# Optimization experiments

Measured on AMD Instinct MI355X. Metric: run time of the kernel, lower is better.

## Reference

```python
import jax, jax.numpy as jnp
import numpy as np

EMBED = 256
HEADS = 8
HD = EMBED // HEADS
LEVELS = 4
POINTS = 4
FFN_H = 1024
BS = 8
LQ = 900
SHAPES = [(100, 100), (50, 50), (25, 25), (13, 13)]


def setup_inputs() -> dict:
    key = jax.random.key(0)
    ks = jax.random.split(key, 20)
    nv = sum(h * w for h, w in SHAPES)
    starts = np.cumsum([0] + [h * w for h, w in SHAPES])[:-1]
    inp = {
        "queries": jax.random.normal(ks[0], (BS, LQ, EMBED), jnp.float32),
        "memory": jax.random.normal(ks[1], (BS, nv, EMBED), jnp.float32),
        "query_pos": jax.random.normal(ks[2], (BS, LQ, EMBED), jnp.float32),
        "reference_points": jax.random.uniform(ks[3], (BS, LQ, LEVELS, 4), jnp.float32) * 0.9 + 0.05,
        "spatial_shapes": jnp.asarray(SHAPES, jnp.int32),
        "level_start_index": jnp.asarray(starts, jnp.int32),
    }
    def lin(k, din, dout):
        k1, k2 = jax.random.split(k)
        w = jax.random.normal(k1, (din, dout), jnp.float32) * 0.02
        b = jax.random.normal(k2, (dout,), jnp.float32) * 0.01
        return w, b
    specs = [("Wq", "bq", EMBED, EMBED), ("Wk", "bk", EMBED, EMBED), ("Wv", "bv", EMBED, EMBED),
             ("Wo", "bo", EMBED, EMBED), ("Wvd", "bvd", EMBED, EMBED),
             ("Woff", "boff", EMBED, HEADS * LEVELS * POINTS * 2),
             ("Watt", "batt", EMBED, HEADS * LEVELS * POINTS),
             ("Wop", "bop", EMBED, EMBED), ("Wg", "bg", 2 * EMBED, 2 * EMBED),
             ("W1", "b1", EMBED, FFN_H), ("W2", "b2", FFN_H, EMBED)]
    for i, (wn, bn, di, do) in enumerate(specs):
        w, b = lin(ks[4 + i], di, do)
        inp[wn] = w
        inp[bn] = b
    for n in ["ln1", "ln2", "ln3"]:
        inp[n + "_s"] = jnp.ones((EMBED,), jnp.float32)
        inp[n + "_b"] = jnp.zeros((EMBED,), jnp.float32)
    return inp


def _ln(x, s, b):
    m = jnp.mean(x, -1, keepdims=True)
    v = jnp.mean(jnp.square(x - m), -1, keepdims=True)
    return (x - m) * jax.lax.rsqrt(v + 1e-5) * s + b


def _bilinear(v_l, lx, ly, H, W):
    # v_l: [bs,h,H*W,hd]; lx,ly: [bs,h,lq,p] normalized in [0,1]
    # grid_sample(align_corners=False, padding=zeros) semantics
    px = lx * W - 0.5
    py = ly * H - 0.5
    x0 = jnp.floor(px)
    y0 = jnp.floor(py)
    wx = px - x0
    wy = py - y0
    x0i = x0.astype(jnp.int32)
    y0i = y0.astype(jnp.int32)
    bs, h, lq, p = lx.shape
    out = jnp.zeros((bs, h, lq, p, HD), v_l.dtype)
    for dy in (0, 1):
        for dx in (0, 1):
            xi = x0i + dx
            yi = y0i + dy
            w = (wx if dx else 1.0 - wx) * (wy if dy else 1.0 - wy)
            valid = (xi >= 0) & (xi < W) & (yi >= 0) & (yi < H)
            idx = jnp.clip(yi, 0, H - 1) * W + jnp.clip(xi, 0, W - 1)
            g = jnp.take_along_axis(v_l, idx.reshape(bs, h, lq * p)[..., None], axis=2)
            g = g.reshape(bs, h, lq, p, HD)
            out = out + w[..., None] * jnp.where(valid[..., None], g, 0.0)
    return out


def reference(queries, memory, query_pos, reference_points, spatial_shapes, level_start_index,
              Wq, bq, Wk, bk, Wv, bv, Wo, bo, Wvd, bvd, Woff, boff, Watt, batt, Wop, bop,
              Wg, bg, W1, b1, W2, b2, ln1_s, ln1_b, ln2_s, ln2_b, ln3_s, ln3_b):
    bs, lq, _ = queries.shape
    shp = np.asarray(spatial_shapes)
    st = np.asarray(level_start_index)

    # ---- self attention (pre-norm, q=k=x+pos, v=x) ----
    x = _ln(queries, ln1_s, ln1_b)
    qk = x + query_pos
    Q = (qk @ Wq + bq).reshape(bs, lq, HEADS, HD)
    K = (qk @ Wk + bk).reshape(bs, lq, HEADS, HD)
    V = (x @ Wv + bv).reshape(bs, lq, HEADS, HD)
    scores = jnp.einsum('bqhd,bkhd->bhqk', Q, K) * (1.0 / np.sqrt(HD))
    attn = jax.nn.softmax(scores, axis=-1)
    sa = jnp.einsum('bhqk,bkhd->bqhd', attn, V).reshape(bs, lq, EMBED) @ Wo + bo
    x1 = queries + sa  # dropout is identity in eval

    # ---- MS-deformable cross attention ----
    y = _ln(x1, ln2_s, ln2_b)
    qc = y + query_pos
    val = (memory @ Wvd + bvd).reshape(bs, -1, HEADS, HD).transpose(0, 2, 1, 3)  # [bs,h,Nv,hd]
    off = (qc @ Woff + boff).reshape(bs, lq, HEADS, LEVELS, POINTS, 2)
    aw = jax.nn.softmax((qc @ Watt + batt).reshape(bs, lq, HEADS, LEVELS * POINTS), axis=-1)
    aw = aw.reshape(bs, lq, HEADS, LEVELS, POINTS)
    rp = reference_points[:, :, None, :, None, :]  # [bs,lq,1,L,1,4]
    loc = rp[..., :2] + off / POINTS * rp[..., 2:] * 0.5  # [bs,lq,h,L,p,2]

    out = jnp.zeros((bs, HEADS, lq, HD), queries.dtype)
    for l in range(LEVELS):
        H, W = int(shp[l, 0]), int(shp[l, 1])
        s0 = int(st[l])
        v_l = val[:, :, s0:s0 + H * W]
        lx = jnp.transpose(loc[:, :, :, l, :, 0], (0, 2, 1, 3))  # [bs,h,lq,p]
        ly = jnp.transpose(loc[:, :, :, l, :, 1], (0, 2, 1, 3))
        samp = _bilinear(v_l, lx, ly, H, W)  # [bs,h,lq,p,hd]
        w = jnp.transpose(aw[:, :, :, l], (0, 2, 1, 3))  # [bs,h,lq,p]
        out = out + jnp.sum(w[..., None] * samp, axis=3)
    cross = out.transpose(0, 2, 1, 3).reshape(bs, lq, EMBED) @ Wop + bop

    # ---- gated fusion ----
    gi = jnp.concatenate([x1, cross], axis=-1)
    g = jax.nn.sigmoid(gi @ Wg + bg)
    x2 = g[..., :EMBED] * x1 + g[..., EMBED:] * cross

    # ---- FFN ----
    z = _ln(x2, ln3_s, ln3_b)
    ffn = jax.nn.relu(z @ W1 + b1) @ W2 + b2
    return (x2 + ffn, aw, loc)
```

## Files before the change

### kernel.cpp

```cpp
#include <hip/hip_runtime.h>
#include <hip/hip_bf16.h>
#include <math.h>

#define BB 8
#define LQ 900
#define EE 256
#define NH 8
#define HD 32
#define NL 4
#define NP 4
#define FFN_H 1024

typedef __bf16 bf16x8 __attribute__((ext_vector_type(8)));
typedef float f32x4 __attribute__((ext_vector_type(4)));
typedef unsigned short u16x8 __attribute__((ext_vector_type(8)));

__device__ __forceinline__ unsigned short f2b(float f) {
    union { float f; unsigned int u; } v; v.f = f;
    unsigned int u = v.u;
    unsigned int r = (u + 0x7fffu + ((u >> 16) & 1u)) >> 16;
    return (unsigned short)r;
}
__device__ __forceinline__ float b2f(unsigned short h) {
    union { unsigned int u; float f; } v; v.u = ((unsigned int)h) << 16; return v.f;
}

typedef __attribute__((address_space(3))) unsigned int* lds_ptr_t;
typedef const __attribute__((address_space(1))) unsigned int* gbl_ptr_t;
#define GLOAD16(g, l) __builtin_amdgcn_global_load_lds((gbl_ptr_t)(g), (lds_ptr_t)(l), 16, 0, 0)
#define VMCNT(n) asm volatile("s_waitcnt vmcnt(" #n ")" ::: "memory")

struct TDesc { const float* src; unsigned short* dst; int K, N, tile0; };
struct TPack {
    TDesc d[12];
    const float *bq, *bk, *boff, *batt;
    float *bqk, *boa;
    const float *Wop_src, *Wg_src, *bop_src, *bg_src;
    unsigned short* WopRow;
    float* bgg;
};

__global__ __launch_bounds__(256) void prep_kernel(
    TPack p,
    const float* __restrict__ queries, const float* __restrict__ qpos,
    const float* __restrict__ ln1_s, const float* __restrict__ ln1_b,
    unsigned short* __restrict__ x_b, unsigned short* __restrict__ qk_b,
    const float* __restrict__ mem, unsigned short* __restrict__ mem_b, long memN)
{
    const int bi = blockIdx.x;
    const int t = threadIdx.x;

    if (bi < 1248) {
        int di = 0;
#pragma unroll
        for (int i = 1; i < 12; ++i) if (bi >= p.d[i].tile0) di = i;
        TDesc d = p.d[di];
        int tt = bi - d.tile0;
        int tn = (d.N + 31) >> 5;
        int tk = tt / tn, tc = tt % tn;
        __shared__ float tile[32][33];
        int tx = t & 31, ty = t >> 5;
#pragma unroll
        for (int i = 0; i < 4; ++i) {
            int kk = tk * 32 + ty + i * 8, nn = tc * 32 + tx;
            tile[ty + i * 8][tx] = d.src[(size_t)kk * d.N + nn];
        }
        __syncthreads();
#pragma unroll
        for (int i = 0; i < 4; ++i) {
            int nn = tc * 32 + ty + i * 8, kk = tk * 32 + tx;
            d.dst[(size_t)nn * d.K + kk] = f2b(tile[tx][ty + i * 8]);
        }
        return;
    }
    if (bi < 1252) {
        int which = bi - 1248;
        if (which == 0)      p.bqk[t] = p.bq[t];
        else if (which == 1) p.bqk[256 + t] = p.bk[t];
        else if (which == 2) p.boa[t] = p.boff[t];
        else if (t < 128)    p.boa[256 + t] = p.batt[t];
        return;
    }
    if (bi < 1284) {
        long i = ((long)(bi - 1252) * 256 + t) * 8;
        float4 a = *(const float4*)(p.Wop_src + i);
        float4 b = *(const float4*)(p.Wop_src + i + 4);
        u16x8 o;
        o[0] = f2b(a.x); o[1] = f2b(a.y); o[2] = f2b(a.z); o[3] = f2b(a.w);
        o[4] = f2b(b.x); o[5] = f2b(b.y); o[6] = f2b(b.z); o[7] = f2b(b.w);
        *(u16x8*)(p.WopRow + i) = o;
        return;
    }
    if (bi < 1286) {
        int n = (bi - 1284) * 256 + t;
        float bb = p.bg_src[n];
        for (int j = 0; j < 256; ++j)
            bb += p.bop_src[j] * p.Wg_src[(size_t)(256 + j) * 512 + n];
        p.bgg[n] = bb;
        return;
    }
    if (bi < 8486) {
        const int row = bi - 1286;
        const int w = t >> 6, lane = t & 63;
        __shared__ float red[4];
        float v = queries[(size_t)row * EE + t];
        float sum = v;
#pragma unroll
        for (int o = 32; o; o >>= 1) sum += __shfl_xor(sum, o, 64);
        if (lane == 0) red[w] = sum;
        __syncthreads();
        float mean = (red[0] + red[1] + red[2] + red[3]) * (1.0f / 256.0f);
        __syncthreads();
        float dd = v - mean;
        float sq = dd * dd;
#pragma unroll
        for (int o = 32; o; o >>= 1) sq += __shfl_xor(sq, o, 64);
        if (lane == 0) red[w] = sq;
        __syncthreads();
        float var = (red[0] + red[1] + red[2] + red[3]) * (1.0f / 256.0f);
        float y = dd * rsqrtf(var + 1e-5f) * ln1_s[t] + ln1_b[t];
        x_b[(size_t)row * EE + t]  = f2b(y);
        qk_b[(size_t)row * EE + t] = f2b(y + qpos[(size_t)row * EE + t]);
        return;
    }
    {
        long i = ((long)(bi - 8486) * 256 + t) * 8;
        long stride = (long)2048 * 256 * 8;
        for (; i < memN; i += stride) {
            float4 a = *(const float4*)(mem + i);
            float4 b = *(const float4*)(mem + i + 4);
            u16x8 o;
            o[0] = f2b(a.x); o[1] = f2b(a.y); o[2] = f2b(a.z); o[3] = f2b(a.w);
            o[4] = f2b(b.x); o[5] = f2b(b.y); o[6] = f2b(b.z); o[7] = f2b(b.w);
            *(u16x8*)(mem_b + i) = o;
        }
    }
}

struct GD {
    const unsigned short* A;
    const unsigned short* Bt;
    const float* bias;
    const float* resid;
    float* outF;
    unsigned short* outB;
    const float* lnS; const float* lnB; const float* lnAdd;
    unsigned short* lnOut;
    int M, K, N, ntN, tile0, ldOutB, outBoff, act, ldA;
};
struct GB { GD d[4]; int nd, tot; };

template<int BN>
__global__ __launch_bounds__(256, (BN == 128) ? 4 : 2) void gemm_pipe(GB g) {
    constexpr int STAGES = (BN == 128) ? 3 : 2;
    __shared__ __align__(16) unsigned short ldsb[STAGES][(64 + BN) * 32];
    __shared__ float lnred[2][64][2];
    const int tid = threadIdx.x;
    const int l = tid & 63, w = tid >> 6;
    const int wr = w >> 1, wc = w & 1;
    constexpr int NJ = BN / 32;

    int t = blockIdx.x;
    if (t >= g.tot) return;
    int d = 0;
    while (d + 1 < g.nd && t >= g.d[d + 1].tile0) ++d;

    auto stage = [&](int dd, int tt, int ks, int pp) {
        const GD& D = g.d[dd];
        const int lda = D.ldA ? D.ldA : D.K;
        int local = tt - D.tile0;
        int m0 = (local / D.ntN) * 64;
        int n0 = (local % D.ntN) * BN;
        unsigned short* base = &ldsb[pp][0];
        {
            int row = w * 16 + (l >> 2);
            int rg = m0 + row; int mm = D.M - 1; rg = rg < mm ? rg : mm;
            int schunk = ((l & 3) ^ ((row >> 1) & 3)) << 4;
            GLOAD16((const char*)(D.A + (size_t)rg * lda + (ks << 5)) + schunk,
                    base + (w * 16) * 32);
        }
#pragma unroll
        for (int ib = 0; ib < BN / 64; ++ib) {
            int row = ib * 64 + w * 16 + (l >> 2);
            int rg = n0 + row; int nn = D.N - 1; rg = rg < nn ? rg : nn;
            int schunk = ((l & 3) ^ ((row >> 1) & 3)) << 4;
            GLOAD16((const char*)(D.Bt + (size_t)rg * D.K + (ks << 5)) + schunk,
                    base + 2048 + (ib * 64 + w * 16) * 32);
        }
    };

    int st_t = t, st_ks = 0, st_d = d;
    bool st_valid = true;
    auto advance = [&]() {
        ++st_ks;
        if (st_ks == (g.d[st_d].K >> 5)) {
            st_ks = 0;
            st_t += gridDim.x;
            if (st_t >= g.tot) { st_valid = false; }
            else { while (st_d + 1 < g.nd && st_t >= g.d[st_d + 1].tile0) ++st_d; }
        }
    };

    int sp = 0, cp = 0, nf = 0;
    stage(st_d, st_t, st_ks, sp); sp = (sp + 1 == STAGES) ? 0 : sp + 1; ++nf; advance();
    if (STAGES == 3 && st_valid) {
        stage(st_d, st_t, st_ks, sp); sp = (sp + 1 == STAGES) ? 0 : sp + 1; ++nf; advance();
    }

    while (true) {
        const GD D = g.d[d];
        int local = t - D.tile0;
        const int m0 = (local / D.ntN) * 64;
        const int n0 = (local % D.ntN) * BN;
        const int nk = D.K >> 5;

        f32x4 acc[2][NJ];
#pragma unroll
        for (int i = 0; i < 2; ++i)
#pragma unroll
            for (int j = 0; j < NJ; ++j) acc[i][j] = (f32x4){0.f, 0.f, 0.f, 0.f};

        for (int ks = 0; ks < nk; ++ks) {
            if (st_valid && nf < STAGES) {
                stage(st_d, st_t, st_ks, sp);
                sp = (sp + 1 == STAGES) ? 0 : sp + 1;
                ++nf; advance();
            }
            if (nf == 3)      { VMCNT(6); }
            else if (nf == 2) { if constexpr (BN == 128) { VMCNT(3); } else { VMCNT(5); } }
            else              { VMCNT(0); }
            __builtin_amdgcn_sched_barrier(0);
            __builtin_amdgcn_s_barrier();
            __builtin_amdgcn_sched_barrier(0);
            {
                const char* base = (const char*)&ldsb[cp][0];
                const int rch = ((l >> 4) ^ ((l >> 1) & 3)) << 4;
                bf16x8 af[2];
#pragma unroll
                for (int i = 0; i < 2; ++i) {
                    int row = wr * 32 + i * 16 + (l & 15);
                    af[i] = *(const bf16x8*)(base + row * 64 + rch);
                }
#pragma unroll
                for (int j = 0; j < NJ; ++j) {
                    int row = wc * (BN / 2) + j * 16 + (l & 15);
                    bf16x8 bfr = *(const bf16x8*)(base + 4096 + row * 64 + rch);
#pragma unroll
                    for (int i = 0; i < 2; ++i)
                        acc[i][j] = __builtin_amdgcn_mfma_f32_16x16x32_bf16(af[i], bfr, acc[i][j], 0, 0, 0);
                }
            }
            __builtin_amdgcn_sched_barrier(0);
            __builtin_amdgcn_s_barrier();
            __builtin_amdgcn_sched_barrier(0);
            cp = (cp + 1 == STAGES) ? 0 : cp + 1;
            --nf;
        }

#pragma unroll
        for (int i = 0; i < 2; ++i) {
#pragma unroll
            for (int r = 0; r < 4; ++r) {
                int gm = m0 + wr * 32 + i * 16 + ((l >> 4) << 2) + r;
                if (gm >= D.M) continue;
#pragma unroll
                for (int j = 0; j < NJ; ++j) {
                    int gn = n0 + wc * (BN / 2) + j * 16 + (l & 15);
                    if (gn >= D.N) continue;
                    float v = acc[i][j][r];
                    if (D.bias)  v += D.bias[gn];
                    if (D.resid) v += D.resid[(size_t)gm * D.N + gn];
                    if (D.act == 1)      v = fmaxf(v, 0.f);
                    else if (D.act == 2) v = 1.0f / (1.0f + __expf(-v));
                    acc[i][j][r] = v;
                    if (D.outF) D.outF[(size_t)gm * D.N + gn] = v;
                    if (D.outB) D.outB[(size_t)gm * D.ldOutB + D.outBoff + gn] = f2b(v);
                }
            }
        }

        if constexpr (BN == 256) {
            if (D.lnOut) {
#pragma unroll
                for (int i = 0; i < 2; ++i) {
#pragma unroll
                    for (int r = 0; r < 4; ++r) {
                        float s1 = 0.f, s2 = 0.f;
#pragma unroll
                        for (int j = 0; j < NJ; ++j) {
                            float v = acc[i][j][r];
                            s1 += v; s2 += v * v;
                        }
#pragma unroll
                        for (int o = 1; o <= 8; o <<= 1) {
                            s1 += __shfl_xor(s1, o, 64);
                            s2 += __shfl_xor(s2, o, 64);
                        }
                        if ((l & 15) == 0) {
                            int row = wr * 32 + i * 16 + ((l >> 4) << 2) + r;
                            lnred[wc][row][0] = s1;
                            lnred[wc][row][1] = s2;
                        }
                    }
                }
                __syncthreads();
#pragma unroll
                for (int i = 0; i < 2; ++i) {
#pragma unroll
                    for (int r = 0; r < 4; ++r) {
                        int row = wr * 32 + i * 16 + ((l >> 4) << 2) + r;
                        int gm = m0 + row;
                        if (gm >= D.M) continue;
                        float mean = (lnred[0][row][0] + lnred[1][row][0]) * (1.0f / 256.0f);
                        float msq  = (lnred[0][row][1] + lnred[1][row][1]) * (1.0f / 256.0f);
                        float rs = rsqrtf(msq - mean * mean + 1e-5f);
#pragma unroll
                        for (int j = 0; j < NJ; ++j) {
                            int gn = wc * 128 + j * 16 + (l & 15);
                            float y = (acc[i][j][r] - mean) * rs * D.lnS[gn] + D.lnB[gn]
                                      + D.lnAdd[(size_t)gm * 256 + gn];
                            D.lnOut[(size_t)gm * 256 + gn] = f2b(y);
                        }
                    }
                }
            }
        }

        t += gridDim.x;
        if (t >= g.tot) break;
        while (d + 1 < g.nd && t >= g.d[d + 1].tile0) ++d;
    }
}

__global__ __launch_bounds__(256) void attn_mfma(
    const unsigned short* __restrict__ QK, const unsigned short* __restrict__ Vb,
    unsigned short* __restrict__ outB)
{
    const int qt = blockIdx.x;
    const int bh = blockIdx.y;
    const int b = bh >> 3, h = bh & 7;
    const int tid = threadIdx.x;
    const int w = tid >> 6, l = tid & 63;

    __shared__ __align__(16) unsigned short Ks[64 * 32];
    __shared__ __align__(16) unsigned short VT[32 * 64];
    __shared__ __align__(16) unsigned short Ps[4][64 * 20];

    const int qrow_w = qt * 64 + w * 16;
    int qr = qrow_w + (l & 15); qr = qr < LQ ? qr : LQ - 1;
    bf16x8 qf = *(const bf16x8*)(QK + ((size_t)(b * LQ + qr)) * 512 + h * 32 + (l >> 4) * 8);

    f32x4 acc0 = {0.f, 0.f, 0.f, 0.f}, acc1 = {0.f, 0.f, 0.f, 0.f};
    float m_run = -1e30f, l_run = 0.f;
    const float scale = 0.17677669529663689f;
    const f32x4 z4 = {0.f, 0.f, 0.f, 0.f};

    const int key = tid >> 2;
    const int dg = (tid & 3) * 8;
    u16x8 kvc, vvc, kvn, vvn;
    {
        int krow = key; krow = krow < LQ ? krow : LQ - 1;
        size_t base = (size_t)(b * LQ + krow);
        kvc = *(const u16x8*)(QK + base * 512 + 256 + h * 32 + dg);
        vvc = *(const u16x8*)(Vb + base * 256 + h * 32 + dg);
    }

    for (int kt = 0; kt < 15; ++kt) {
        __syncthreads();
        *(u16x8*)((char*)Ks + key * 64 + ((dg * 2) ^ ((key & 3) << 4))) = kvc;
#pragma unroll
        for (int e = 0; e < 8; ++e) {
            int dd = dg + e;
            *(unsigned short*)((char*)VT + dd * 128 + ((key * 2) ^ ((dd & 7) << 4))) = vvc[e];
        }
        if (kt < 14) {
            int krow = (kt + 1) * 64 + key; krow = krow < LQ ? krow : LQ - 1;
            size_t base = (size_t)(b * LQ + krow);
            kvn = *(const u16x8*)(QK + base * 512 + 256 + h * 32 + dg);
            vvn = *(const u16x8*)(Vb + base * 256 + h * 32 + dg);
        }
        __syncthreads();

        float p[4][4];
        float tmax = -1e30f;
#pragma unroll
        for (int m = 0; m < 4; ++m) {
            int kr = m * 16 + (l & 15);
            bf16x8 kf = *(const bf16x8*)((const char*)Ks + kr * 64 +
                        (((l >> 4) * 16) ^ ((kr & 3) << 4)));
            f32x4 sf = __builtin_amdgcn_mfma_f32_16x16x32_bf16(kf, qf, z4, 0, 0, 0);
#pragma unroll
            for (int r = 0; r < 4; ++r) {
                int kk = kt * 64 + m * 16 + (l >> 4) * 4 + r;
                float sv = (kk < LQ) ? sf[r] * scale : -1e30f;
                p[m][r] = sv;
                tmax = fmaxf(tmax, sv);
            }
        }
        tmax = fmaxf(tmax, __shfl_xor(tmax, 16, 64));
        tmax = fmaxf(tmax, __shfl_xor(tmax, 32, 64));
        float newm = fmaxf(m_run, tmax);
        float corr = __expf(m_run - newm);
        m_run = newm;
        float tsum = 0.f;
#pragma unroll
        for (int m = 0; m < 4; ++m)
#pragma unroll
            for (int r = 0; r < 4; ++r) {
                float e = __expf(p[m][r] - newm);
                p[m][r] = e;
                tsum += e;
            }
        tsum += __shfl_xor(tsum, 16, 64);
        tsum += __shfl_xor(tsum, 32, 64);
        l_run = l_run * corr + tsum;
        acc0 *= corr;
        acc1 *= corr;

        unsigned short* pw = &Ps[w][0];
#pragma unroll
        for (int m = 0; m < 4; ++m)
#pragma unroll
            for (int r = 0; r < 4; ++r) {
                int kk = m * 16 + (l >> 4) * 4 + r;
                pw[kk * 20 + (l & 15)] = f2b(p[m][r]);
            }

#pragma unroll
        for (int s = 0; s < 2; ++s) {
            union { unsigned short u[8]; bf16x8 v; } pb;
#pragma unroll
            for (int j = 0; j < 8; ++j)
                pb.u[j] = pw[(s * 32 + (l >> 4) * 8 + j) * 20 + (l & 15)];
#pragma unroll
            for (int m2 = 0; m2 < 2; ++m2) {
                int dd = m2 * 16 + (l & 15);
                bf16x8 vf = *(const bf16x8*)((const char*)VT + dd * 128 +
                            ((s * 64 + (l >> 4) * 16) ^ ((dd & 7) << 4)));
                if (m2 == 0) acc0 = __builtin_amdgcn_mfma_f32_16x16x32_bf16(vf, pb.v, acc0, 0, 0, 0);
                else         acc1 = __builtin_amdgcn_mfma_f32_16x16x32_bf16(vf, pb.v, acc1, 0, 0, 0);
            }
        }
        if (kt < 14) { kvc = kvn; vvc = vvn; }
    }

    float inv = 1.0f / l_run;
    int q = qrow_w + (l & 15);
    if (q < LQ) {
        size_t obase = ((size_t)(b * LQ + q)) * 256 + h * 32;
#pragma unroll
        for (int r = 0; r < 4; ++r) {
            int d0 = (l >> 4) * 4 + r;
            outB[obase + d0]      = f2b(acc0[r] * inv);
            outB[obase + 16 + d0] = f2b(acc1[r] * inv);
        }
    }
}

__global__ __launch_bounds__(256) void sample_fused(
    const float* __restrict__ off_att, const float* __restrict__ refp,
    const unsigned short* __restrict__ val,
    const int* __restrict__ shapes, const int* __restrict__ starts,
    float* __restrict__ aw_out, float* __restrict__ loc_out,
    unsigned short* __restrict__ xs, int NV)
{
    const int row = blockIdx.x;
    const int b = row / LQ;
    const int t = threadIdx.x;
    const int h = t >> 5, d = t & 31;

    __shared__ float l_logit[128];
    __shared__ float l_aw[128];
    __shared__ float l_loc[256];
    __shared__ int l_sh[NL * 2];
    __shared__ int l_st[NL];

    if (t < 128) l_logit[t] = off_att[(size_t)row * 384 + 256 + t];
    {
        float o = off_att[(size_t)row * 384 + t];
        int c = t & 1;
        int lv = (t >> 3) & 3;
        float rc = refp[((size_t)row * 4 + lv) * 4 + c];
        float rs = refp[((size_t)row * 4 + lv) * 4 + 2 + c];
        float loc = rc + o * 0.125f * rs;
        l_loc[t] = loc;
        loc_out[(size_t)row * 256 + t] = loc;
    }
    if (t < NL * 2) l_sh[t] = shapes[t];
    if (t < NL) l_st[t] = starts[t];
    __syncthreads();
    if (t < 128) {
        int hh = t >> 4;
        float mx = -1e30f;
#pragma unroll
        for (int i = 0; i < 16; ++i) mx = fmaxf(mx, l_logit[hh * 16 + i]);
        float sum = 0.f;
#pragma unroll
        for (int i = 0; i < 16; ++i) sum += __expf(l_logit[hh * 16 + i] - mx);
        float aw = __expf(l_logit[t] - mx) / sum;
        l_aw[t] = aw;
        aw_out[(size_t)row * 128 + t] = aw;
    }
    __syncthreads();

    float acc = 0.f;
    const unsigned short* vb = val + (size_t)b * NV * EE + h * HD + d;

#pragma unroll
    for (int lv = 0; lv < NL; ++lv) {
        const int Hh = l_sh[lv * 2], Ww = l_sh[lv * 2 + 1];
        const int s0 = l_st[lv];
#pragma unroll
        for (int p = 0; p < NP; ++p) {
            const int base = ((h * NL + lv) * NP + p) * 2;
            float lx = l_loc[base], ly = l_loc[base + 1];
            float wgt0 = l_aw[h * 16 + lv * NP + p];
            float px = lx * (float)Ww - 0.5f;
            float py = ly * (float)Hh - 0.5f;
            float x0f = floorf(px), y0f = floorf(py);
            float wx = px - x0f, wy = py - y0f;
            int x0 = (int)x0f, y0 = (int)y0f;
#pragma unroll
            for (int dy = 0; dy < 2; ++dy) {
                int yi = y0 + dy;
                bool vy = (yi >= 0) && (yi < Hh);
                int yc = min(max(yi, 0), Hh - 1);
                float wyv = dy ? wy : 1.f - wy;
#pragma unroll
                for (int dx = 0; dx < 2; ++dx) {
                    int xi = x0 + dx;
                    bool vv = vy && (xi >= 0) && (xi < Ww);
                    int xc = min(max(xi, 0), Ww - 1);
                    float wgt = wgt0 * wyv * (dx ? wx : 1.f - wx);
                    float gv = b2f(vb[(size_t)(s0 + yc * Ww + xc) * EE]);
                    acc += vv ? wgt * gv : 0.f;
                }
            }
        }
    }
    xs[(size_t)row * 512 + 256 + t] = f2b(acc);
}

__global__ __launch_bounds__(256) void gate_ln3(
    const float* __restrict__ g, const float* __restrict__ x1,
    const float* __restrict__ cross, const float* __restrict__ s,
    const float* __restrict__ bln, float* __restrict__ x2out,
    unsigned short* __restrict__ zb)
{
    const int row = blockIdx.x;
    const int t = threadIdx.x;
    const int w = t >> 6;
    const int lane = t & 63;
    __shared__ float red[4];

    float g1 = g[(size_t)row * 512 + t];
    float g2 = g[(size_t)row * 512 + 256 + t];
    float v = g1 * x1[(size_t)row * EE + t] + g2 * cross[(size_t)row * EE + t];
    x2out[(size_t)row * EE + t] = v;

    float sum = v;
#pragma unroll
    for (int o = 32; o; o >>= 1) sum += __shfl_xor(sum, o, 64);
    if (lane == 0) red[w] = sum;
    __syncthreads();
    float mean = (red[0] + red[1] + red[2] + red[3]) * (1.0f / 256.0f);
    __syncthreads();

    float d = v - mean;
    float sq = d * d;
#pragma unroll
    for (int o = 32; o; o >>= 1) sq += __shfl_xor(sq, o, 64);
    if (lane == 0) red[w] = sq;
    __syncthreads();
    float var = (red[0] + red[1] + red[2] + red[3]) * (1.0f / 256.0f);

    float y = d * rsqrtf(var + 1e-5f) * s[t] + bln[t];
    zb[(size_t)row * EE + t] = f2b(y);
}

extern "C" void kernel_launch(void* const* d_in, const int* in_sizes, int n_in,
                              void* d_out, int out_size, void* d_ws, size_t ws_size,
                              hipStream_t stream)
{
    const float* queries   = (const float*)d_in[0];
    const float* memory    = (const float*)d_in[1];
    const float* query_pos = (const float*)d_in[2];
    const float* refp      = (const float*)d_in[3];
    const int*   shapes    = (const int*)d_in[4];
    const int*   starts    = (const int*)d_in[5];
    const float* Wq  = (const float*)d_in[6],  *bq  = (const float*)d_in[7];
    const float* Wk  = (const float*)d_in[8],  *bk  = (const float*)d_in[9];
    const float* Wv  = (const float*)d_in[10], *bv  = (const float*)d_in[11];
    const float* Wo  = (const float*)d_in[12], *bo  = (const float*)d_in[13];
    const float* Wvd = (const float*)d_in[14], *bvd = (const float*)d_in[15];
    const float* Woff= (const float*)d_in[16], *boff= (const float*)d_in[17];
    const float* Watt= (const float*)d_in[18], *batt= (const float*)d_in[19];
    const float* Wop = (const float*)d_in[20], *bop = (const float*)d_in[21];
    const float* Wg  = (const float*)d_in[22], *bg  = (const float*)d_in[23];
    const float* W1  = (const float*)d_in[24], *b1  = (const float*)d_in[25];
    const float* W2  = (const float*)d_in[26], *b2  = (const float*)d_in[27];
    const float* ln1_s = (const float*)d_in[28], *ln1_b = (const float*)d_in[29];
    const float* ln2_s = (const float*)d_in[30], *ln2_b = (const float*)d_in[31];
    const float* ln3_s = (const float*)d_in[32], *ln3_b = (const float*)d_in[33];

    const int NV = in_sizes[1] / (BB * EE);
    const int Mq = BB * LQ;
    const int Mv = BB * NV;
    const long memN = (long)Mv * EE;

    char* W8 = (char*)d_ws;
    size_t off = 0;
    auto alloc = [&](size_t bytes) { char* p = W8 + off; off += (bytes + 255) & ~(size_t)255; return p; };

    unsigned short* mem_b = (unsigned short*)alloc((size_t)memN * 2);
    unsigned short* val_b = (unsigned short*)alloc((size_t)memN * 2);
    unsigned short* WtQK  = (unsigned short*)alloc(512 * 256 * 2);
    unsigned short* WtV   = (unsigned short*)alloc(256 * 256 * 2);
    unsigned short* WtO   = (unsigned short*)alloc(256 * 256 * 2);
    unsigned short* WtVD  = (unsigned short*)alloc(256 * 256 * 2);
    unsigned short* WtOA  = (unsigned short*)alloc(384 * 256 * 2);
    unsigned short* WtOP  = (unsigned short*)alloc(256 * 256 * 2);
    unsigned short* WtGF  = (unsigned short*)alloc(512 * 512 * 2);
    unsigned short* Wg2T  = (unsigned short*)alloc(512 * 256 * 2);
    unsigned short* WopRow= (unsigned short*)alloc(256 * 256 * 2);
    unsigned short* Wt1   = (unsigned short*)alloc(1024 * 256 * 2);
    unsigned short* Wt2   = (unsigned short*)alloc(256 * 1024 * 2);
    float*          bqk   = (float*)alloc(512 * 4);
    float*          boa   = (float*)alloc(384 * 4);
    float*          bgg   = (float*)alloc(512 * 4);
    unsigned short* qkb   = (unsigned short*)alloc((size_t)Mq * 512 * 2);
    unsigned short* vb_buf= (unsigned short*)alloc((size_t)Mq * 256 * 2);
    unsigned short* av_buf= (unsigned short*)alloc((size_t)Mq * 256 * 2);
    float*          x1    = (float*)alloc((size_t)Mq * 256 * 4);
    unsigned short* xs_cat= (unsigned short*)alloc((size_t)Mq * 512 * 2);
    unsigned short* qc_b  = (unsigned short*)alloc((size_t)Mq * 256 * 2);
    unsigned short* qk_b  = (unsigned short*)alloc((size_t)Mq * 256 * 2);
    float*          cross = (float*)alloc((size_t)Mq * 256 * 4);

    unsigned short* x_b = (unsigned short*)cross;
    float* off_att = (float*)qkb;
    float* gbuf = (float*)mem_b;
    float* x2   = (float*)((char*)mem_b + (size_t)Mq * 512 * 4);
    unsigned short* z_b = (unsigned short*)((char*)x2 + (size_t)Mq * 256 * 4);
    unsigned short* hidden_b = (unsigned short*)((char*)z_b + (size_t)Mq * 256 * 2);

    float* out0    = (float*)d_out;
    float* aw_out  = out0 + (size_t)Mq * 256;
    float* loc_out = aw_out + (size_t)Mq * 128;

    dim3 blk(256);
    const int tMq = (Mq + 63) / 64;
    const int tv  = (Mv + 63) / 64;

    TPack tp;
    tp.d[0]  = { Wq,             WtQK,             256, 256,    0 };
    tp.d[1]  = { Wk,             WtQK + 256 * 256, 256, 256,   64 };
    tp.d[2]  = { Wv,             WtV,              256, 256,  128 };
    tp.d[3]  = { Wo,             WtO,              256, 256,  192 };
    tp.d[4]  = { Wvd,            WtVD,             256, 256,  256 };
    tp.d[5]  = { Woff,           WtOA,             256, 256,  320 };
    tp.d[6]  = { Watt,           WtOA + 256 * 256, 256, 128,  384 };
    tp.d[7]  = { Wop,            WtOP,             256, 256,  416 };
    tp.d[8]  = { Wg,             WtGF,             512, 512,  480 };
    tp.d[9]  = { Wg + 256 * 512, Wg2T,             256, 512,  608 };
    tp.d[10] = { W1,             Wt1,              256, 1024, 736 };
    tp.d[11] = { W2,             Wt2,             1024, 256,  992 };
    tp.bq = bq; tp.bk = bk; tp.boff = boff; tp.batt = batt;
    tp.bqk = bqk; tp.boa = boa;
    tp.Wop_src = Wop; tp.Wg_src = Wg; tp.bop_src = bop; tp.bg_src = bg;
    tp.WopRow = WopRow; tp.bgg = bgg;
    prep_kernel<<<10534, blk, 0, stream>>>(
        tp, queries, query_pos, ln1_s, ln1_b, x_b, qk_b, memory, mem_b, memN);

    {
        GB g; g.nd = 4;
        g.d[0] = { mem_b, WtVD, bvd, nullptr, nullptr, val_b,
                   nullptr, nullptr, nullptr, nullptr,
                   Mv, 256, 256, 2, 0, 256, 0, 0, 0 };
        g.d[1] = { qk_b, WtQK, bqk, nullptr, nullptr, qkb,
                   nullptr, nullptr, nullptr, nullptr,
                   Mq, 256, 512, 4, tv * 2, 512, 0, 0, 0 };
        g.d[2] = { x_b, WtV, bv, nullptr, nullptr, vb_buf,
                   nullptr, nullptr, nullptr, nullptr,
                   Mq, 256, 256, 2, tv * 2 + tMq * 4, 256, 0, 0, 0 };
        g.d[3] = { Wg2T, WopRow, nullptr, nullptr, nullptr, WtGF,
                   nullptr, nullptr, nullptr, nullptr,
                   512, 256, 256, 2, tv * 2 + tMq * 6, 512, 256, 0, 0 };
        g.tot = tv * 2 + tMq * 6 + 16;
        gemm_pipe<128><<<1536, blk, 0, stream>>>(g);
    }

    attn_mfma<<<dim3(15, BB * NH), blk, 0, stream>>>(qkb, vb_buf, av_buf);

    {
        GB g; g.nd = 1;
        g.d[0] = { av_buf, WtO, bo, queries, x1, xs_cat,
                   ln2_s, ln2_b, query_pos, qc_b,
                   Mq, 256, 256, 1, 0, 512, 0, 0, 0 };
        g.tot = tMq;
        gemm_pipe<256><<<tMq, blk, 0, stream>>>(g);
    }

    {
        GB g; g.nd = 1;
        g.d[0] = { qc_b, WtOA, boa, nullptr, off_att, nullptr,
                   nullptr, nullptr, nullptr, nullptr,
                   Mq, 256, 384, 3, 0, 384, 0, 0, 0 };
        g.tot = tMq * 3;
        gemm_pipe<128><<<g.tot, blk, 0, stream>>>(g);
    }

    sample_fused<<<Mq, blk, 0, stream>>>(off_att, refp, val_b, shapes, starts,
                                         aw_out, loc_out, xs_cat, NV);

    {
        GB g; g.nd = 2;
        g.d[0] = { xs_cat + 256, WtOP, bop, nullptr, cross, nullptr,
                   nullptr, nullptr, nullptr, nullptr,
                   Mq, 256, 256, 2, 0, 0, 0, 0, 512 };
        g.d[1] = { xs_cat, WtGF, bgg, nullptr, gbuf, nullptr,
                   nullptr, nullptr, nullptr, nullptr,
                   Mq, 512, 512, 4, tMq * 2, 0, 0, 2, 0 };
        g.tot = tMq * 6;
        gemm_pipe<128><<<g.tot, blk, 0, stream>>>(g);
    }

    gate_ln3<<<Mq, blk, 0, stream>>>(gbuf, x1, cross, ln3_s, ln3_b, x2, z_b);

    {
        GB g; g.nd = 1;
        g.d[0] = { z_b, Wt1, b1, nullptr, nullptr, hidden_b,
                   nullptr, nullptr, nullptr, nullptr,
                   Mq, 256, 1024, 8, 0, 1024, 0, 1, 0 };
        g.tot = tMq * 8;
        gemm_pipe<128><<<g.tot, blk, 0, stream>>>(g);
    }

    {
        GB g; g.nd = 1;
        g.d[0] = { hidden_b, Wt2, b2, x2, out0, nullptr,
                   nullptr, nullptr, nullptr, nullptr,
                   Mq, 1024, 256, 2, 0, 256, 0, 0, 0 };
        g.tot = tMq * 2;
        gemm_pipe<128><<<g.tot, blk, 0, stream>>>(g);
    }
}
```

Measured before the change: 346.4 us.

## Co-schedule value projection GEMM with self-attention kernel and simplify GEMM pipeline

The large memory value-projection GEMM moves out of the batched projection launch and into the self-attention launch. Extra blocks in that launch run it as a persistent double-buffered GEMM, so it overlaps with the attention blocks instead of sitting ahead of them. The generic GEMM kernel drops its 3-stage cross-tile prefetch for a simpler 2-stage double buffer. This cuts LDS use and may raise occupancy, but it risks less latency hiding. Shared memory in the attention kernel is merged into one buffer that both block roles reuse.

```diff
diff --git a/kernel.cpp b/kernel.cpp
--- a/kernel.cpp
+++ b/kernel.cpp
@@ -148,12 +148,11 @@
     unsigned short* lnOut;
     int M, K, N, ntN, tile0, ldOutB, outBoff, act, ldA;
 };
-struct GB { GD d[4]; int nd, tot; };
+struct GB { GD d[3]; int nd, tot; };
 
 template<int BN>
 __global__ __launch_bounds__(256, (BN == 128) ? 4 : 2) void gemm_pipe(GB g) {
-    constexpr int STAGES = (BN == 128) ? 3 : 2;
-    __shared__ __align__(16) unsigned short ldsb[STAGES][(64 + BN) * 32];
+    __shared__ __align__(16) unsigned short ldsb[2][(64 + BN) * 32];
     __shared__ float lnred[2][64][2];
     const int tid = threadIdx.x;
     const int l = tid & 63, w = tid >> 6;
@@ -189,23 +188,8 @@
         }
     };
 
-    int st_t = t, st_ks = 0, st_d = d;
-    bool st_valid = true;
-    auto advance = [&]() {
-        ++st_ks;
-        if (st_ks == (g.d[st_d].K >> 5)) {
-            st_ks = 0;
-            st_t += gridDim.x;
-            if (st_t >= g.tot) { st_valid = false; }
-            else { while (st_d + 1 < g.nd && st_t >= g.d[st_d + 1].tile0) ++st_d; }
-        }
-    };
-
-    int sp = 0, cp = 0, nf = 0;
-    stage(st_d, st_t, st_ks, sp); sp = (sp + 1 == STAGES) ? 0 : sp + 1; ++nf; advance();
-    if (STAGES == 3 && st_valid) {
-        stage(st_d, st_t, st_ks, sp); sp = (sp + 1 == STAGES) ? 0 : sp + 1; ++nf; advance();
-    }
+    stage(d, t, 0, 0);
+    int p = 0;
 
     while (true) {
         const GD D = g.d[d];
@@ -221,19 +205,24 @@
             for (int j = 0; j < NJ; ++j) acc[i][j] = (f32x4){0.f, 0.f, 0.f, 0.f};
 
         for (int ks = 0; ks < nk; ++ks) {
-            if (st_valid && nf < STAGES) {
-                stage(st_d, st_t, st_ks, sp);
-                sp = (sp + 1 == STAGES) ? 0 : sp + 1;
-                ++nf; advance();
-            }
-            if (nf == 3)      { VMCNT(6); }
-            else if (nf == 2) { if constexpr (BN == 128) { VMCNT(3); } else { VMCNT(5); } }
-            else              { VMCNT(0); }
+            int nt = t, nks = ks + 1, ndd = d;
+            bool have = true;
+            if (nks == nk) {
+                nt = t + gridDim.x; nks = 0;
+                if (nt >= g.tot) have = false;
+                else { while (ndd + 1 < g.nd && nt >= g.d[ndd + 1].tile0) ++ndd; }
+            }
+            if (have) {
+                stage(ndd, nt, nks, p ^ 1);
+                if constexpr (BN == 128) { VMCNT(3); } else { VMCNT(5); }
+            } else {
+                VMCNT(0);
+            }
             __builtin_amdgcn_sched_barrier(0);
             __builtin_amdgcn_s_barrier();
             __builtin_amdgcn_sched_barrier(0);
             {
-                const char* base = (const char*)&ldsb[cp][0];
+                const char* base = (const char*)&ldsb[p][0];
                 const int rch = ((l >> 4) ^ ((l >> 1) & 3)) << 4;
                 bf16x8 af[2];
 #pragma unroll
@@ -253,8 +242,7 @@
             __builtin_amdgcn_sched_barrier(0);
             __builtin_amdgcn_s_barrier();
             __builtin_amdgcn_sched_barrier(0);
-            cp = (cp + 1 == STAGES) ? 0 : cp + 1;
-            --nf;
+            p ^= 1;
         }
 
 #pragma unroll
@@ -332,19 +320,122 @@
     }
 }
 
-__global__ __launch_bounds__(256) void attn_mfma(
+#define VGRID 1536
+
+__global__ __launch_bounds__(256) void attn_val(
     const unsigned short* __restrict__ QK, const unsigned short* __restrict__ Vb,
-    unsigned short* __restrict__ outB)
+    unsigned short* __restrict__ outB,
+    const unsigned short* __restrict__ vA, const unsigned short* __restrict__ vBt,
+    const float* __restrict__ vbias, unsigned short* __restrict__ vout,
+    int Mv, int vtiles)
 {
-    const int qt = blockIdx.x;
-    const int bh = blockIdx.y;
+    __shared__ __align__(16) unsigned short smem[(64 + 128) * 32 * 2];
+    const int bid = blockIdx.x;
+    const int tid = threadIdx.x;
+    const int l = tid & 63, w = tid >> 6;
+
+    if (bid >= 960) {
+        const int wr = w >> 1, wc = w & 1;
+        int t = bid - 960;
+        if (t >= vtiles) return;
+
+        auto stage = [&](int tt, int ks, int pp) {
+            unsigned short* base = &smem[pp * 192 * 32];
+            int m0 = (tt >> 1) * 64;
+            int n0 = (tt & 1) * 128;
+            {
+                int row = w * 16 + (l >> 2);
+                int rg = m0 + row; int mm = Mv - 1; rg = rg < mm ? rg : mm;
+                int schunk = ((l & 3) ^ ((row >> 1) & 3)) << 4;
+                GLOAD16((const char*)(vA + (size_t)rg * 256 + (ks << 5)) + schunk,
+                        base + (w * 16) * 32);
+            }
+#pragma unroll
+            for (int ib = 0; ib < 2; ++ib) {
+                int row = ib * 64 + w * 16 + (l >> 2);
+                int rg = n0 + row;
+                int schunk = ((l & 3) ^ ((row >> 1) & 3)) << 4;
+                GLOAD16((const char*)(vBt + (size_t)rg * 256 + (ks << 5)) + schunk,
+                        base + 2048 + (ib * 64 + w * 16) * 32);
+            }
+        };
+
+        stage(t, 0, 0);
+        int p = 0;
+        while (true) {
+            const int m0 = (t >> 1) * 64;
+            const int n0 = (t & 1) * 128;
+
+            f32x4 acc[2][4];
+#pragma unroll
+            for (int i = 0; i < 2; ++i)
+#pragma unroll
+                for (int j = 0; j < 4; ++j) acc[i][j] = (f32x4){0.f, 0.f, 0.f, 0.f};
+
+            for (int ks = 0; ks < 8; ++ks) {
+                int nt = t, nks = ks + 1;
+                bool have = true;
+                if (nks == 8) {
+                    nt = t + VGRID; nks = 0;
+                    if (nt >= vtiles) have = false;
+                }
+                if (have) { stage(nt, nks, p ^ 1); VMCNT(3); }
+                else      { VMCNT(0); }
+                __builtin_amdgcn_sched_barrier(0);
+                __builtin_amdgcn_s_barrier();
+                __builtin_amdgcn_sched_barrier(0);
+                {
+                    const char* base = (const char*)&smem[p * 192 * 32];
+                    const int rch = ((l >> 4) ^ ((l >> 1) & 3)) << 4;
+                    bf16x8 af[2];
+#pragma unroll
+                    for (int i = 0; i < 2; ++i) {
+                        int row = wr * 32 + i * 16 + (l & 15);
+                        af[i] = *(const bf16x8*)(base + row * 64 + rch);
+                    }
+#pragma unroll
+                    for (int j = 0; j < 4; ++j) {
+                        int row = wc * 64 + j * 16 + (l & 15);
+                        bf16x8 bfr = *(const bf16x8*)(base + 4096 + row * 64 + rch);
+#pragma unroll
+                        for (int i = 0; i < 2; ++i)
+                            acc[i][j] = __builtin_amdgcn_mfma_f32_16x16x32_bf16(af[i], bfr, acc[i][j], 0, 0, 0);
+                    }
+                }
+                __builtin_amdgcn_sched_barrier(0);
+                __builtin_amdgcn_s_barrier();
+                __builtin_amdgcn_sched_barrier(0);
+                p ^= 1;
+            }
+
+#pragma unroll
+            for (int i = 0; i < 2; ++i) {
+#pragma unroll
+                for (int r = 0; r < 4; ++r) {
+                    int gm = m0 + wr * 32 + i * 16 + ((l >> 4) << 2) + r;
+                    if (gm >= Mv) continue;
+#pragma unroll
+                    for (int j = 0; j < 4; ++j) {
+                        int gn = n0 + wc * 64 + j * 16 + (l & 15);
+                        float v = acc[i][j][r] + vbias[gn];
+                        vout[(size_t)gm * 256 + gn] = f2b(v);
+                    }
+                }
+            }
+
+            t += VGRID;
+            if (t >= vtiles) break;
+        }
+        return;
+    }
+
+    const int qt = bid % 15;
+    const int bh = bid / 15;
     const int b = bh >> 3, h = bh & 7;
-    const int tid = threadIdx.x;
-    const int w = tid >> 6, l = tid & 63;
-
-    __shared__ __align__(16) unsigned short Ks[64 * 32];
-    __shared__ __align__(16) unsigned short VT[32 * 64];
-    __shared__ __align__(16) unsigned short Ps[4][64 * 20];
+
+    unsigned short* Ks = smem;
+    unsigned short* VT = smem + 2048;
+    unsigned short* Ps = smem + 4096;
 
     const int qrow_w = qt * 64 + w * 16;
     int qr = qrow_w + (l & 15); qr = qr < LQ ? qr : LQ - 1;
@@ -381,7 +472,7 @@
         }
         __syncthreads();
 
-        float p[4][4];
+        float pv[4][4];
         float tmax = -1e30f;
 #pragma unroll
         for (int m = 0; m < 4; ++m) {
@@ -393,7 +484,7 @@
             for (int r = 0; r < 4; ++r) {
                 int kk = kt * 64 + m * 16 + (l >> 4) * 4 + r;
                 float sv = (kk < LQ) ? sf[r] * scale : -1e30f;
-                p[m][r] = sv;
+                pv[m][r] = sv;
                 tmax = fmaxf(tmax, sv);
             }
         }
@@ -407,8 +498,8 @@
         for (int m = 0; m < 4; ++m)
 #pragma unroll
             for (int r = 0; r < 4; ++r) {
-                float e = __expf(p[m][r] - newm);
-                p[m][r] = e;
+                float e = __expf(pv[m][r] - newm);
+                pv[m][r] = e;
                 tsum += e;
             }
         tsum += __shfl_xor(tsum, 16, 64);
@@ -417,13 +508,13 @@
         acc0 *= corr;
         acc1 *= corr;
 
-        unsigned short* pw = &Ps[w][0];
+        unsigned short* pw = Ps + w * 1280;
 #pragma unroll
         for (int m = 0; m < 4; ++m)
 #pragma unroll
             for (int r = 0; r < 4; ++r) {
                 int kk = m * 16 + (l >> 4) * 4 + r;
-                pw[kk * 20 + (l & 15)] = f2b(p[m][r]);
+                pw[kk * 20 + (l & 15)] = f2b(pv[m][r]);
             }
 
 #pragma unroll
@@ -673,24 +764,22 @@
         tp, queries, query_pos, ln1_s, ln1_b, x_b, qk_b, memory, mem_b, memN);
 
     {
-        GB g; g.nd = 4;
-        g.d[0] = { mem_b, WtVD, bvd, nullptr, nullptr, val_b,
+        GB g; g.nd = 3;
+        g.d[0] = { qk_b, WtQK, bqk, nullptr, nullptr, qkb,
                    nullptr, nullptr, nullptr, nullptr,
-                   Mv, 256, 256, 2, 0, 256, 0, 0, 0 };
-        g.d[1] = { qk_b, WtQK, bqk, nullptr, nullptr, qkb,
+                   Mq, 256, 512, 4, 0, 512, 0, 0, 0 };
+        g.d[1] = { x_b, WtV, bv, nullptr, nullptr, vb_buf,
                    nullptr, nullptr, nullptr, nullptr,
-                   Mq, 256, 512, 4, tv * 2, 512, 0, 0, 0 };
-        g.d[2] = { x_b, WtV, bv, nullptr, nullptr, vb_buf,
+                   Mq, 256, 256, 2, tMq * 4, 256, 0, 0, 0 };
+        g.d[2] = { Wg2T, WopRow, nullptr, nullptr, nullptr, WtGF,
                    nullptr, nullptr, nullptr, nullptr,
-                   Mq, 256, 256, 2, tv * 2 + tMq * 4, 256, 0, 0, 0 };
-        g.d[3] = { Wg2T, WopRow, nullptr, nullptr, nullptr, WtGF,
-                   nullptr, nullptr, nullptr, nullptr,
-                   512, 256, 256, 2, tv * 2 + tMq * 6, 512, 256, 0, 0 };
-        g.tot = tv * 2 + tMq * 6 + 16;
-        gemm_pipe<128><<<1536, blk, 0, stream>>>(g);
-    }
-
-    attn_mfma<<<dim3(15, BB * NH), blk, 0, stream>>>(qkb, vb_buf, av_buf);
+                   512, 256, 256, 2, tMq * 6, 512, 256, 0, 0 };
+        g.tot = tMq * 6 + 16;
+        gemm_pipe<128><<<g.tot, blk, 0, stream>>>(g);
+    }
+
+    attn_val<<<960 + VGRID, blk, 0, stream>>>(
+        qkb, vb_buf, av_buf, mem_b, WtVD, bvd, val_b, Mv, tv * 2);
 
     {
         GB g; g.nd = 1;
```

After: 303.9 us. 1.14x faster.
